# Kernel optimization log

Measured on AMD Instinct MI355X. Metric: run time of the kernel, lower is better.

The kernel has to match this reference:

```python
import jax, jax.numpy as jnp
import numpy as np


def _conv(x, w, pad):
    return jax.lax.conv_general_dilated(x, w, (1, 1), [(pad, pad), (pad, pad)],
                                        dimension_numbers=('NCHW', 'OIHW', 'NCHW'))


def _cbs(x, w, s, b, pad):
    # Conv + (folded inference BatchNorm as per-channel affine) + SiLU
    y = _conv(x, w, pad) * s[None, :, None, None] + b[None, :, None, None]
    return y * jax.nn.sigmoid(y)


def _pixel_shuffle(x, r):
    N, C, H, W = x.shape
    c = C // (r * r)
    return x.reshape(N, c, r, r, H, W).transpose(0, 1, 4, 2, 5, 3).reshape(N, c, H * r, W * r)


def _pixel_unshuffle(x, r):
    N, C, H, W = x.shape
    h, w = H // r, W // r
    return x.reshape(N, C, h, r, w, r).transpose(0, 1, 3, 5, 2, 4).reshape(N, C * r * r, h, w)


def _carafe(x, dw, db, ew, eb, k, up):
    # Content-aware reassembly: predict per-pixel k*k kernels for up*up sub-positions,
    # softmax-normalize, then gather-multiply-accumulate over k*k neighborhoods.
    N, C, H, W = x.shape
    kt = _conv(x, dw, 0) + db[None, :, None, None]
    if k % 2 == 0:
        kt = jnp.pad(kt, ((0, 0), (0, 0), (k // 2, k // 2 - 1), (k // 2, k // 2 - 1)))
        kt = _conv(kt, ew, 0) + eb[None, :, None, None]
    else:
        kt = _conv(kt, ew, k // 2) + eb[None, :, None, None]
    kt = _pixel_shuffle(kt, up)                     # [N, k*k, H*up, W*up]
    kt = jax.nn.softmax(kt, axis=1)
    # non-overlapping unfold(step=up) -> [N, H, W, k*k, up*up]
    kt = kt.reshape(N, k * k, H, up, W, up).transpose(0, 2, 4, 1, 3, 5).reshape(N, H, W, k * k, up * up)
    if k % 2 == 0:
        xp = jnp.pad(x, ((0, 0), (0, 0), (k // 2, k // 2 - 1), (k // 2, k // 2 - 1)))
    else:
        xp = jnp.pad(x, ((0, 0), (0, 0), (k // 2, k // 2), (k // 2, k // 2)))
    # k*k sliding patches (k is a small static constant)
    patches = jnp.stack([xp[:, :, i:i + H, j:j + W] for i in range(k) for j in range(k)], axis=-1)
    patches = patches.transpose(0, 2, 3, 1, 4)      # [N, H, W, C, k*k]
    out = jnp.einsum('nhwck,nhwkr->nhwcr', patches, kt)  # [N, H, W, C, up*up]
    out = out.reshape(N, H, W, C * up * up).transpose(0, 3, 1, 2)
    return _pixel_shuffle(out, up)


def _forward(x, cv1_w, cv1_s, cv1_b, m1a_w, m1a_s, m1a_b, m1b_w, m1b_s, m1b_b,
             cvm2_w, cvm2_s, cvm2_b, u2_down_w, u2_down_b, u2_enc_w, u2_enc_b,
             m2a_w, m2a_s, m2a_b, m2b_w, m2b_s, m2b_b,
             cvm3_w, cvm3_s, cvm3_b, u3_down_w, u3_down_b, u3_enc_w, u3_enc_b,
             m3a_w, m3a_s, m3a_b, m3b_w, m3b_s, m3b_b, cv2_w, cv2_s, cv2_b):
    C = cv1_w.shape[0] // 2
    t = _cbs(x, cv1_w, cv1_s, cv1_b, 0)
    y, y0 = t[:, :C], t[:, C:]

    def bneck(z, wa, sa, ba, wb, sb, bb):  # shortcut=False, e=1.0
        return _cbs(_cbs(z, wa, sa, ba, 1), wb, sb, bb, 1)

    y1 = bneck(y0, m1a_w, m1a_s, m1a_b, m1b_w, m1b_s, m1b_b)
    y2 = _cbs(_pixel_unshuffle(y1, 2), cvm2_w, cvm2_s, cvm2_b, 0)
    y2 = _carafe(y2, u2_down_w, u2_down_b, u2_enc_w, u2_enc_b, 1, 2) + y1
    y2 = bneck(y2, m2a_w, m2a_s, m2a_b, m2b_w, m2b_s, m2b_b)
    y3 = _cbs(_pixel_unshuffle(y2, 4), cvm3_w, cvm3_s, cvm3_b, 0)
    y3 = _carafe(y3, u3_down_w, u3_down_b, u3_enc_w, u3_enc_b, 2, 4) + y2
    y3 = bneck(y3, m3a_w, m3a_s, m3a_b, m3b_w, m3b_s, m3b_b)
    return _cbs(jnp.concatenate([y, y0, y1, y2, y3], axis=1), cv2_w, cv2_s, cv2_b, 0)


def setup_inputs() -> dict:
    key = jax.random.key(0)
    ks = jax.random.split(key, 16)
    C = 128

    def cbs_p(k, co, ci, ksz):
        k1, k2, k3 = jax.random.split(k, 3)
        w = jax.random.normal(k1, (co, ci, ksz, ksz), jnp.float32) / np.sqrt(ci * ksz * ksz).astype(np.float32)
        s = 1.0 + 0.1 * jax.random.normal(k2, (co,), jnp.float32)
        b = 0.1 * jax.random.normal(k3, (co,), jnp.float32)
        return w, s, b

    d = {}
    d['x'] = jax.random.normal(ks[0], (8, 256, 128, 128), jnp.float32)
    d['cv1_w'], d['cv1_s'], d['cv1_b'] = cbs_p(ks[1], 2 * C, 256, 1)
    for name, kk in (('m1', ks[2]), ('m2', ks[3]), ('m3', ks[4])):
        ka, kb = jax.random.split(kk)
        d[name + 'a_w'], d[name + 'a_s'], d[name + 'a_b'] = cbs_p(ka, C, C, 3)
        d[name + 'b_w'], d[name + 'b_s'], d[name + 'b_b'] = cbs_p(kb, C, C, 3)
    d['cvm2_w'], d['cvm2_s'], d['cvm2_b'] = cbs_p(ks[5], C, 4 * C, 1)
    d['cvm3_w'], d['cvm3_s'], d['cvm3_b'] = cbs_p(ks[6], C, 16 * C, 1)
    d['u2_down_w'] = jax.random.normal(ks[7], (C // 4, C, 1, 1), jnp.float32) / np.sqrt(C).astype(np.float32)
    d['u2_down_b'] = 0.1 * jax.random.normal(ks[8], (C // 4,), jnp.float32)
    d['u2_enc_w'] = jax.random.normal(ks[9], (4, C // 4, 1, 1), jnp.float32) / np.sqrt(C // 4).astype(np.float32)
    d['u2_enc_b'] = 0.1 * jax.random.normal(ks[10], (4,), jnp.float32)
    d['u3_down_w'] = jax.random.normal(ks[11], (C // 4, C, 1, 1), jnp.float32) / np.sqrt(C).astype(np.float32)
    d['u3_down_b'] = 0.1 * jax.random.normal(ks[12], (C // 4,), jnp.float32)
    d['u3_enc_w'] = jax.random.normal(ks[13], (64, C // 4, 2, 2), jnp.float32) / np.sqrt((C // 4) * 4).astype(np.float32)
    d['u3_enc_b'] = 0.1 * jax.random.normal(ks[14], (64,), jnp.float32)
    d['cv2_w'], d['cv2_s'], d['cv2_b'] = cbs_p(ks[15], 256, 5 * C, 1)
    return d


def reference(x, cv1_w, cv1_s, cv1_b, m1a_w, m1a_s, m1a_b, m1b_w, m1b_s, m1b_b,
              cvm2_w, cvm2_s, cvm2_b, u2_down_w, u2_down_b, u2_enc_w, u2_enc_b,
              m2a_w, m2a_s, m2a_b, m2b_w, m2b_s, m2b_b,
              cvm3_w, cvm3_s, cvm3_b, u3_down_w, u3_down_b, u3_enc_w, u3_enc_b,
              m3a_w, m3a_s, m3a_b, m3b_w, m3b_s, m3b_b, cv2_w, cv2_s, cv2_b):
    return _forward(x, cv1_w, cv1_s, cv1_b, m1a_w, m1a_s, m1a_b, m1b_w, m1b_s, m1b_b,
                    cvm2_w, cvm2_s, cvm2_b, u2_down_w, u2_down_b, u2_enc_w, u2_enc_b,
                    m2a_w, m2a_s, m2a_b, m2b_w, m2b_s, m2b_b,
                    cvm3_w, cvm3_s, cvm3_b, u3_down_w, u3_down_b, u3_enc_w, u3_enc_b,
                    m3a_w, m3a_s, m3a_b, m3b_w, m3b_s, m3b_b, cv2_w, cv2_s, cv2_b)
```

## Files before the change

kernel.cpp:

```cpp
#include <hip/hip_runtime.h>

typedef unsigned short u16;
typedef short v8s __attribute__((ext_vector_type(8)));
typedef u16 v8u __attribute__((ext_vector_type(8)));
typedef float v4f __attribute__((ext_vector_type(4)));
typedef __bf16 v8bf __attribute__((ext_vector_type(8)));

__device__ __forceinline__ float bf2f(u16 u) {
    unsigned x = ((unsigned)u) << 16; float f; __builtin_memcpy(&f, &x, 4); return f;
}
__device__ __forceinline__ u16 f2bf(float f) {
    unsigned x; __builtin_memcpy(&x, &f, 4);
    x = x + 0x7FFFu + ((x >> 16) & 1u);
    return (u16)(x >> 16);
}
__device__ __forceinline__ float silu(float v) { return v / (1.f + __expf(-v)); }

__device__ __forceinline__ void gld16(const void* g, void* l) {
    __builtin_amdgcn_global_load_lds(
        (const __attribute__((address_space(1))) unsigned int*)(uintptr_t)g,
        (__attribute__((address_space(3))) unsigned int*)(unsigned int)(uintptr_t)l,
        16, 0, 0);
}

__global__ void cvtw(const float* __restrict__ in, u16* __restrict__ out, int n) {
    int i = blockIdx.x * 256 + threadIdx.x;
    if (i < n) out[i] = f2bf(in[i]);
}
__global__ void wtrans3(const float* __restrict__ in, u16* __restrict__ out) {
    int i = blockIdx.x * 256 + threadIdx.x;
    if (i >= 147456) return;
    int tap = i % 9; int rem = i / 9; int ci = rem & 127; int co = rem >> 7;
    out[((tap * 128 + co) << 7) + ci] = f2bf(in[i]);
}
__global__ void wtrans_ps(const float* __restrict__ in, u16* __restrict__ out, int R2) {
    int i = blockIdx.x * 256 + threadIdx.x;
    int tap = i % R2; int rem = i / R2; int c = rem & 127; int co = rem >> 7;
    out[((tap * 128 + co) << 7) + c] = f2bf(in[i]);
}

__global__ __launch_bounds__(256) void nchw2nhwc(const float* __restrict__ in, u16* __restrict__ out) {
    __shared__ u16 tile[64][72];
    const int n = blockIdx.z, c0 = blockIdx.y * 64, p0 = blockIdx.x * 64;
#pragma unroll
    for (int rep = 0; rep < 16; ++rep) {
        int idx = rep * 256 + threadIdx.x;
        int c = idx >> 6, p = idx & 63;
        tile[c][p] = f2bf(in[((size_t)(n * 256 + c0 + c)) * 16384 + p0 + p]);
    }
    __syncthreads();
#pragma unroll
    for (int rep = 0; rep < 16; ++rep) {
        int idx = rep * 256 + threadIdx.x;
        int p = idx >> 6, c = idx & 63;
        out[((size_t)n * 16384 + p0 + p) * 256 + c0 + c] = tile[c][p];
    }
}

__global__ __launch_bounds__(256) void conv3_mfma(
    const u16* __restrict__ src, int c0, int srcC,
    const u16* __restrict__ wt,
    const float* __restrict__ scale, const float* __restrict__ bias,
    u16* __restrict__ out) {
    __shared__ u16 lds[3][128][32];
    const int n = blockIdx.y, h = blockIdx.x;
    const int tid = threadIdx.x;
    const int lane = tid & 63;
    const int wv = tid >> 6;
    const int r = lane & 15, q = lane >> 4;
    const int wr = wv >> 1, wc = wv & 1;

    v4f acc[4][4];
#pragma unroll
    for (int a = 0; a < 4; ++a)
#pragma unroll
        for (int b = 0; b < 4; ++b) acc[a][b] = (v4f){0.f, 0.f, 0.f, 0.f};

    const size_t rowstride = (size_t)128 * srcC;
    const u16* nbase = src + (size_t)n * 128 * rowstride + c0;

    for (int k0 = 0; k0 < 128; k0 += 32) {
        __syncthreads();
#pragma unroll
        for (int kh = 0; kh < 3; ++kh) {
            int hh = h + kh - 1;
            if ((unsigned)hh < 128u) {
                const u16* g = nbase + (size_t)hh * rowstride + k0;
#pragma unroll
                for (int j = 0; j < 2; ++j) {
                    int o = j * 4096 + tid * 16;
                    int px = o >> 6, cb = o & 63;
                    gld16((const char*)(g + (size_t)px * srcC) + cb,
                          (char*)&lds[kh][0][0] + j * 4096 + wv * 1024);
                }
            }
        }
        __syncthreads();
#pragma unroll
        for (int kh = 0; kh < 3; ++kh) {
            int hh = h + kh - 1;
            if ((unsigned)hh >= 128u) continue;
#pragma unroll
            for (int kw = 0; kw < 3; ++kw) {
                int tap = kh * 3 + kw;
                const u16* bb = wt + ((size_t)tap * 128 + wc * 64 + r) * 128 + k0 + q * 8;
                v8bf bfr[4];
#pragma unroll
                for (int nt = 0; nt < 4; ++nt)
                    bfr[nt] = __builtin_bit_cast(v8bf, *(const v8s*)(bb + nt * 16 * 128));
                v8bf afr[4];
#pragma unroll
                for (int mt = 0; mt < 4; ++mt) {
                    int p = wr * 64 + mt * 16 + r + kw - 1;
                    bool vp = (unsigned)p < 128u;
                    int pc = vp ? p : 0;
                    v8s av = *(const v8s*)&lds[kh][pc][q * 8];
                    if (!vp) av = (v8s){0, 0, 0, 0, 0, 0, 0, 0};
                    afr[mt] = __builtin_bit_cast(v8bf, av);
                }
#pragma unroll
                for (int mt = 0; mt < 4; ++mt)
#pragma unroll
                    for (int nt = 0; nt < 4; ++nt)
                        acc[mt][nt] = __builtin_amdgcn_mfma_f32_16x16x32_bf16(
                            afr[mt], bfr[nt], acc[mt][nt], 0, 0, 0);
            }
        }
    }

    const size_t obase = ((size_t)n * 128 + h) * 128;
#pragma unroll
    for (int nt = 0; nt < 4; ++nt) {
        int co = wc * 64 + nt * 16 + r;
        float s = scale[co], bi = bias[co];
#pragma unroll
        for (int mt = 0; mt < 4; ++mt) {
            int p = wr * 64 + mt * 16 + q * 4;
#pragma unroll
            for (int i = 0; i < 4; ++i) {
                float v = acc[mt][nt][i] * s + bi;
                out[(obase + p + i) * 128 + co] = f2bf(silu(v));
            }
        }
    }
}

__global__ __launch_bounds__(256) void conv1_mfma(
    const u16* __restrict__ src, int srcC,
    const u16* __restrict__ wt,
    const float* __restrict__ scale, const float* __restrict__ bias,
    u16* __restrict__ out, int Cout) {
    __shared__ u16 lds[128][64];
    const int n = blockIdx.z, co0 = blockIdx.y * 128, px0 = blockIdx.x * 128;
    const int tid = threadIdx.x;
    const int lane = tid & 63, wv = tid >> 6;
    const int r = lane & 15, q = lane >> 4;
    const int wr = wv >> 1, wc = wv & 1;

    v4f acc[4][4];
#pragma unroll
    for (int a = 0; a < 4; ++a)
#pragma unroll
        for (int b = 0; b < 4; ++b) acc[a][b] = (v4f){0.f, 0.f, 0.f, 0.f};

    const u16* abase = src + ((size_t)n * 16384 + px0) * srcC;

    for (int k0 = 0; k0 < srcC; k0 += 64) {
        __syncthreads();
#pragma unroll
        for (int j = 0; j < 4; ++j) {
            int o = j * 4096 + tid * 16;
            int px = o >> 7, cb = o & 127;
            gld16((const char*)(abase + (size_t)px * srcC + k0) + cb,
                  (char*)&lds[0][0] + j * 4096 + wv * 1024);
        }
        __syncthreads();
#pragma unroll
        for (int s = 0; s < 2; ++s) {
            const u16* bb = wt + (size_t)(co0 + wc * 64 + r) * srcC + k0 + s * 32 + q * 8;
            v8bf bfr[4];
#pragma unroll
            for (int nt = 0; nt < 4; ++nt)
                bfr[nt] = __builtin_bit_cast(v8bf, *(const v8s*)(bb + (size_t)nt * 16 * srcC));
            v8bf afr[4];
#pragma unroll
            for (int mt = 0; mt < 4; ++mt)
                afr[mt] = __builtin_bit_cast(v8bf, *(const v8s*)&lds[wr * 64 + mt * 16 + r][s * 32 + q * 8]);
#pragma unroll
            for (int mt = 0; mt < 4; ++mt)
#pragma unroll
                for (int nt = 0; nt < 4; ++nt)
                    acc[mt][nt] = __builtin_amdgcn_mfma_f32_16x16x32_bf16(
                        afr[mt], bfr[nt], acc[mt][nt], 0, 0, 0);
        }
    }

#pragma unroll
    for (int nt = 0; nt < 4; ++nt) {
        int co = co0 + wc * 64 + nt * 16 + r;
        float s = scale[co], bi = bias[co];
#pragma unroll
        for (int mt = 0; mt < 4; ++mt) {
            int p = px0 + wr * 64 + mt * 16 + q * 4;
#pragma unroll
            for (int i = 0; i < 4; ++i) {
                float v = acc[mt][nt][i] * s + bi;
                out[((size_t)n * 16384 + p + i) * Cout + co] = f2bf(silu(v));
            }
        }
    }
}

__global__ __launch_bounds__(256) void cat_mfma(
    const u16* __restrict__ s0, const u16* __restrict__ s1,
    const u16* __restrict__ s2, const u16* __restrict__ s3,
    const u16* __restrict__ wt,
    const float* __restrict__ scale, const float* __restrict__ bias,
    float* __restrict__ out) {
    __shared__ u16 lds[128][64];
    const int n = blockIdx.z, co0 = blockIdx.y * 128, px0 = blockIdx.x * 128;
    const int tid = threadIdx.x;
    const int lane = tid & 63, wv = tid >> 6;
    const int r = lane & 15, q = lane >> 4;
    const int wr = wv >> 1, wc = wv & 1;

    v4f acc[4][4];
#pragma unroll
    for (int a = 0; a < 4; ++a)
#pragma unroll
        for (int b = 0; b < 4; ++b) acc[a][b] = (v4f){0.f, 0.f, 0.f, 0.f};

    const u16* srcs[4] = {s0, s1, s2, s3};
    const int sCq[4] = {256, 128, 128, 128};
    const int kbq[4] = {0, 256, 384, 512};

#pragma unroll
    for (int seg = 0; seg < 4; ++seg) {
        const int sc = sCq[seg];
        const u16* ab = srcs[seg] + ((size_t)n * 16384 + px0) * sc;
        for (int k0 = 0; k0 < sc; k0 += 64) {
            __syncthreads();
#pragma unroll
            for (int j = 0; j < 4; ++j) {
                int o = j * 4096 + tid * 16;
                int px = o >> 7, cb = o & 127;
                gld16((const char*)(ab + (size_t)px * sc + k0) + cb,
                      (char*)&lds[0][0] + j * 4096 + wv * 1024);
            }
            __syncthreads();
#pragma unroll
            for (int s = 0; s < 2; ++s) {
                const u16* bb = wt + (size_t)(co0 + wc * 64 + r) * 640 + kbq[seg] + k0 + s * 32 + q * 8;
                v8bf bfr[4];
#pragma unroll
                for (int nt = 0; nt < 4; ++nt)
                    bfr[nt] = __builtin_bit_cast(v8bf, *(const v8s*)(bb + nt * 16 * 640));
                v8bf afr[4];
#pragma unroll
                for (int mt = 0; mt < 4; ++mt)
                    afr[mt] = __builtin_bit_cast(v8bf, *(const v8s*)&lds[wr * 64 + mt * 16 + r][s * 32 + q * 8]);
#pragma unroll
                for (int mt = 0; mt < 4; ++mt)
#pragma unroll
                    for (int nt = 0; nt < 4; ++nt)
                        acc[mt][nt] = __builtin_amdgcn_mfma_f32_16x16x32_bf16(
                            afr[mt], bfr[nt], acc[mt][nt], 0, 0, 0);
            }
        }
    }

#pragma unroll
    for (int nt = 0; nt < 4; ++nt) {
        int co = co0 + wc * 64 + nt * 16 + r;
        float s = scale[co], bi = bias[co];
#pragma unroll
        for (int mt = 0; mt < 4; ++mt) {
            int p = px0 + wr * 64 + mt * 16 + q * 4;
            v4f o;
#pragma unroll
            for (int i = 0; i < 4; ++i) o[i] = silu(acc[mt][nt][i] * s + bi);
            *(v4f*)(out + (size_t)(n * 256 + co) * 16384 + p) = o;
        }
    }
}

template <int KH, int KW, int S, int PAD, int CIN>
__global__ __launch_bounds__(256) void conv_mfma(
    const u16* __restrict__ src, int c0, int srcC,
    const u16* __restrict__ wt,
    const float* __restrict__ scale, const float* __restrict__ bias,
    u16* __restrict__ out, int Hin, int Win, int Wout, int Cout) {
    const int n = blockIdx.z;
    const int co0 = blockIdx.y * 64;
    const int hw0 = blockIdx.x * 64;
    const int tid = threadIdx.x;
    const int lane = tid & 63, wv = tid >> 6;
    const int r = lane & 15, q = lane >> 4;
    const int wr = wv >> 1, wc = wv & 1;

    const int m0 = hw0 + wr * 32 + r;
    const int m1 = m0 + 16;
    const int h0 = m0 / Wout, w0 = m0 - h0 * Wout;
    const int h1 = m1 / Wout, w1 = m1 - h1 * Wout;

    v4f acc00 = {0.f, 0.f, 0.f, 0.f}, acc01 = {0.f, 0.f, 0.f, 0.f};
    v4f acc10 = {0.f, 0.f, 0.f, 0.f}, acc11 = {0.f, 0.f, 0.f, 0.f};

    const u16* b0base = wt + (size_t)(co0 + wc * 32 + r) * CIN + q * 8;
    const size_t wtap = (size_t)Cout * CIN;

    int tap = 0;
#pragma unroll
    for (int kh = 0; kh < KH; ++kh)
#pragma unroll
        for (int kw = 0; kw < KW; ++kw, ++tap) {
            int ih0 = h0 * S + kh - PAD, iw0 = w0 * S + kw - PAD;
            int ih1 = h1 * S + kh - PAD, iw1 = w1 * S + kw - PAD;
            bool v0 = ((unsigned)ih0 < (unsigned)Hin) & ((unsigned)iw0 < (unsigned)Win);
            bool v1 = ((unsigned)ih1 < (unsigned)Hin) & ((unsigned)iw1 < (unsigned)Win);
            int p0i = v0 ? (n * Hin + ih0) * Win + iw0 : 0;
            int p1i = v1 ? (n * Hin + ih1) * Win + iw1 : 0;
            const u16* a0 = src + (size_t)p0i * srcC + c0 + q * 8;
            const u16* a1 = src + (size_t)p1i * srcC + c0 + q * 8;
            const u16* b0 = b0base + (size_t)tap * wtap;
            const u16* b1 = b0 + (size_t)16 * CIN;
#pragma unroll
            for (int k = 0; k < CIN; k += 32) {
                v8s za = {0, 0, 0, 0, 0, 0, 0, 0};
                v8s a0s = za, a1s = za;
                if (v0) a0s = *(const v8s*)(a0 + k);
                if (v1) a1s = *(const v8s*)(a1 + k);
                v8s b0s = *(const v8s*)(b0 + k);
                v8s b1s = *(const v8s*)(b1 + k);
                v8bf af0 = __builtin_bit_cast(v8bf, a0s);
                v8bf af1 = __builtin_bit_cast(v8bf, a1s);
                v8bf bw0 = __builtin_bit_cast(v8bf, b0s);
                v8bf bw1 = __builtin_bit_cast(v8bf, b1s);
                acc00 = __builtin_amdgcn_mfma_f32_16x16x32_bf16(af0, bw0, acc00, 0, 0, 0);
                acc01 = __builtin_amdgcn_mfma_f32_16x16x32_bf16(af0, bw1, acc01, 0, 0, 0);
                acc10 = __builtin_amdgcn_mfma_f32_16x16x32_bf16(af1, bw0, acc10, 0, 0, 0);
                acc11 = __builtin_amdgcn_mfma_f32_16x16x32_bf16(af1, bw1, acc11, 0, 0, 0);
            }
        }

    const int HWo = gridDim.x * 64;
#pragma unroll
    for (int ct = 0; ct < 2; ++ct) {
        v4f av0 = ct ? acc01 : acc00;
        v4f av1 = ct ? acc11 : acc10;
        int co = co0 + wc * 32 + ct * 16 + r;
        float s = scale[co], bb = bias[co];
        int mb = hw0 + wr * 32 + q * 4;
#pragma unroll
        for (int i = 0; i < 4; ++i) {
            float x0 = av0[i] * s + bb;
            float x1 = av1[i] * s + bb;
            out[((size_t)n * HWo + mb + i) * Cout + co] = f2bf(silu(x0));
            out[((size_t)n * HWo + mb + 16 + i) * Cout + co] = f2bf(silu(x1));
        }
    }
}

__global__ __launch_bounds__(256) void k_upadd(const u16* __restrict__ y2a,
                                               const u16* __restrict__ y1,
                                               u16* __restrict__ out) {
    int t = blockIdx.x * 256 + threadIdx.x;
    int cg = t & 15; int pix = t >> 4;
    int n = pix >> 14; int p = pix & 16383; int ho = p >> 7; int wo = p & 127;
    const u16* a = y2a + ((size_t)((n * 64 + (ho >> 1)) * 64 + (wo >> 1))) * 128 + cg * 8;
    const u16* b = y1 + (size_t)pix * 128 + cg * 8;
    v8s av = *(const v8s*)a;
    v8s bv = *(const v8s*)b;
    v8u o;
#pragma unroll
    for (int e = 0; e < 8; ++e) o[e] = f2bf(bf2f((u16)av[e]) + bf2f((u16)bv[e]));
    *(v8u*)(out + (size_t)pix * 128 + cg * 8) = o;
}

__global__ __launch_bounds__(256) void k_u3down(const u16* __restrict__ y3a,
                                                const float* __restrict__ w,
                                                const float* __restrict__ b,
                                                float* __restrict__ ktA) {
    int t = blockIdx.x * 256 + threadIdx.x;
    int co = t & 31; int pix = t >> 5;
    const u16* xr = y3a + (size_t)pix * 128;
    const float* wr = w + (size_t)co * 128;
    float acc = b[co];
#pragma unroll 16
    for (int k = 0; k < 128; ++k) acc += bf2f(xr[k]) * wr[k];
    ktA[t] = acc;
}

__global__ __launch_bounds__(256) void k_u3enc(const float* __restrict__ ktA,
                                               const float* __restrict__ ew,
                                               const float* __restrict__ eb,
                                               float* __restrict__ wtsm) {
    int t = blockIdx.x * 256 + threadIdx.x;
    int r = t & 15; int pix = t >> 4;
    int n = pix >> 10; int hw = pix & 1023; int h = hw >> 5; int w = hw & 31;
    float v[4];
#pragma unroll
    for (int kk = 0; kk < 4; ++kk) {
        int co = kk * 16 + r;
        float acc = eb[co];
#pragma unroll
        for (int dh = 0; dh < 2; ++dh)
#pragma unroll
            for (int dw = 0; dw < 2; ++dw) {
                int hh = h - 1 + dh, ww = w - 1 + dw;
                if (hh < 0 || ww < 0) continue;
                const float* kp = ktA + ((size_t)((n * 32 + hh) * 32 + ww)) * 32;
                const float* wp = ew + (size_t)co * 128 + dh * 2 + dw;
                for (int ci = 0; ci < 32; ++ci) acc += kp[ci] * wp[ci * 4];
            }
        v[kk] = acc;
    }
    float mx = fmaxf(fmaxf(v[0], v[1]), fmaxf(v[2], v[3]));
    float e0 = __expf(v[0] - mx), e1 = __expf(v[1] - mx), e2 = __expf(v[2] - mx), e3 = __expf(v[3] - mx);
    float inv = 1.f / (e0 + e1 + e2 + e3);
    float* o = wtsm + (size_t)t * 4;
    o[0] = e0 * inv; o[1] = e1 * inv; o[2] = e2 * inv; o[3] = e3 * inv;
}

__global__ __launch_bounds__(256) void k_carafe(const u16* __restrict__ y3a,
                                                const float* __restrict__ wtsm,
                                                const u16* __restrict__ y2,
                                                u16* __restrict__ out) {
    int t = blockIdx.x * 256 + threadIdx.x;
    int cg = t & 15; int pix = t >> 4;
    int n = pix >> 14; int p = pix & 16383; int ho = p >> 7; int wo = p & 127;
    int h = ho >> 2, i = ho & 3, w = wo >> 2, j = wo & 3, r = i * 4 + j;
    const float* wv = wtsm + ((size_t)((n * 1024 + h * 32 + w) * 16 + r)) * 4;
    v8s yv = *(const v8s*)(y2 + (size_t)pix * 128 + cg * 8);
    float acc[8];
#pragma unroll
    for (int e = 0; e < 8; ++e) acc[e] = bf2f((u16)yv[e]);
#pragma unroll
    for (int kk = 0; kk < 4; ++kk) {
        int ki = kk >> 1, kj = kk & 1;
        int hh = h + ki - 1, ww = w + kj - 1;
        if (hh < 0 || ww < 0) continue;
        float wk = wv[kk];
        v8s sv = *(const v8s*)(y3a + ((size_t)((n * 32 + hh) * 32 + ww)) * 128 + cg * 8);
#pragma unroll
        for (int e = 0; e < 8; ++e) acc[e] += wk * bf2f((u16)sv[e]);
    }
    v8u o;
#pragma unroll
    for (int e = 0; e < 8; ++e) o[e] = f2bf(acc[e]);
    *(v8u*)(out + (size_t)pix * 128 + cg * 8) = o;
}

extern "C" void kernel_launch(void* const* d_in, const int* in_sizes, int n_in,
                              void* d_out, int out_size, void* d_ws, size_t ws_size,
                              hipStream_t stream) {
    const float* x     = (const float*)d_in[0];
    const float* cv1_w = (const float*)d_in[1];
    const float* cv1_s = (const float*)d_in[2];
    const float* cv1_b = (const float*)d_in[3];
    const float* m1a_w = (const float*)d_in[4];
    const float* m1a_s = (const float*)d_in[5];
    const float* m1a_b = (const float*)d_in[6];
    const float* m1b_w = (const float*)d_in[7];
    const float* m1b_s = (const float*)d_in[8];
    const float* m1b_b = (const float*)d_in[9];
    const float* m2a_w = (const float*)d_in[10];
    const float* m2a_s = (const float*)d_in[11];
    const float* m2a_b = (const float*)d_in[12];
    const float* m2b_w = (const float*)d_in[13];
    const float* m2b_s = (const float*)d_in[14];
    const float* m2b_b = (const float*)d_in[15];
    const float* m3a_w = (const float*)d_in[16];
    const float* m3a_s = (const float*)d_in[17];
    const float* m3a_b = (const float*)d_in[18];
    const float* m3b_w = (const float*)d_in[19];
    const float* m3b_s = (const float*)d_in[20];
    const float* m3b_b = (const float*)d_in[21];
    const float* cvm2_w = (const float*)d_in[22];
    const float* cvm2_s = (const float*)d_in[23];
    const float* cvm2_b = (const float*)d_in[24];
    const float* cvm3_w = (const float*)d_in[25];
    const float* cvm3_s = (const float*)d_in[26];
    const float* cvm3_b = (const float*)d_in[27];
    const float* u3_down_w = (const float*)d_in[32];
    const float* u3_down_b = (const float*)d_in[33];
    const float* u3_enc_w  = (const float*)d_in[34];
    const float* u3_enc_b  = (const float*)d_in[35];
    const float* cv2_w = (const float*)d_in[36];
    const float* cv2_s = (const float*)d_in[37];
    const float* cv2_b = (const float*)d_in[38];

    char* ws = (char*)d_ws;
    u16* A    = (u16*)(ws + 0);
    u16* t    = (u16*)(ws + 67108864);
    u16* y1   = (u16*)(ws + 134217728);
    u16* bt   = (u16*)(ws + 167772160);
    u16* te   = (u16*)(ws + 201326592);
    u16* y2a  = (u16*)(ws + 234881024);
    u16* y3a  = (u16*)(ws + 243269632);
    float* ktA = (float*)(ws + 245366784);
    float* wts = (float*)(ws + 246415360);
    u16* w3t  = (u16*)(ws + 248512512);
    u16* wu2  = (u16*)(ws + 250281984);
    u16* wu4  = (u16*)(ws + 250413056);
    u16* wc1  = (u16*)(ws + 250937344);
    u16* wc2  = (u16*)(ws + 251068416);
    u16* y2 = A;
    u16* y3 = A + 16777216;

    dim3 B(256);
    wtrans3<<<576, B, 0, stream>>>(m1a_w, w3t + 0 * 147456);
    wtrans3<<<576, B, 0, stream>>>(m1b_w, w3t + 1 * 147456);
    wtrans3<<<576, B, 0, stream>>>(m2a_w, w3t + 2 * 147456);
    wtrans3<<<576, B, 0, stream>>>(m2b_w, w3t + 3 * 147456);
    wtrans3<<<576, B, 0, stream>>>(m3a_w, w3t + 4 * 147456);
    wtrans3<<<576, B, 0, stream>>>(m3b_w, w3t + 5 * 147456);
    wtrans_ps<<<256, B, 0, stream>>>(cvm2_w, wu2, 4);
    wtrans_ps<<<1024, B, 0, stream>>>(cvm3_w, wu4, 16);
    cvtw<<<256, B, 0, stream>>>(cv1_w, wc1, 65536);
    cvtw<<<640, B, 0, stream>>>(cv2_w, wc2, 163840);

    nchw2nhwc<<<dim3(256, 4, 8), B, 0, stream>>>(x, A);

    conv1_mfma<<<dim3(128, 2, 8), B, 0, stream>>>(A, 256, wc1, cv1_s, cv1_b, t, 256);

    conv3_mfma<<<dim3(128, 8), B, 0, stream>>>(t, 128, 256, w3t + 0 * 147456, m1a_s, m1a_b, bt);
    conv3_mfma<<<dim3(128, 8), B, 0, stream>>>(bt, 0, 128, w3t + 1 * 147456, m1b_s, m1b_b, y1);

    conv_mfma<2, 2, 2, 0, 128><<<dim3(64, 2, 8), B, 0, stream>>>(
        y1, 0, 128, wu2, cvm2_s, cvm2_b, y2a, 128, 128, 64, 128);

    k_upadd<<<8192, B, 0, stream>>>(y2a, y1, te);

    conv3_mfma<<<dim3(128, 8), B, 0, stream>>>(te, 0, 128, w3t + 2 * 147456, m2a_s, m2a_b, bt);
    conv3_mfma<<<dim3(128, 8), B, 0, stream>>>(bt, 0, 128, w3t + 3 * 147456, m2b_s, m2b_b, y2);

    conv_mfma<4, 4, 4, 0, 128><<<dim3(16, 2, 8), B, 0, stream>>>(
        y2, 0, 128, wu4, cvm3_s, cvm3_b, y3a, 128, 128, 32, 128);

    k_u3down<<<1024, B, 0, stream>>>(y3a, u3_down_w, u3_down_b, ktA);
    k_u3enc<<<512, B, 0, stream>>>(ktA, u3_enc_w, u3_enc_b, wts);
    k_carafe<<<8192, B, 0, stream>>>(y3a, wts, y2, te);

    conv3_mfma<<<dim3(128, 8), B, 0, stream>>>(te, 0, 128, w3t + 4 * 147456, m3a_s, m3a_b, bt);
    conv3_mfma<<<dim3(128, 8), B, 0, stream>>>(bt, 0, 128, w3t + 5 * 147456, m3b_s, m3b_b, y3);

    cat_mfma<<<dim3(128, 2, 8), B, 0, stream>>>(t, y1, y2, y3, wc2, cv2_s, cv2_b, (float*)d_out);
}
```

Baseline: 1.383 ms.

## Double-buffer LDS tiles with XOR swizzle and prefetch weights in MFMA conv kernels

Adds double-buffered LDS staging to the 3x3, 1x1 and concat-conv MFMA kernels, so the next K-chunk's global-to-LDS load is issued while the current chunk is computed. LDS addresses get an XOR swizzle to avoid bank conflicts on fragment reads. The 3x3 kernel prefetches next-tap weights into registers, and out-of-range rows are zero-filled in LDS. This doubles LDS use and raises register pressure, and a launch-bounds occupancy hint is added. There is only one barrier per iteration, which could race when the next stage overwrites a buffer still being read.

```diff
diff --git a/kernel.cpp b/kernel.cpp
--- a/kernel.cpp
+++ b/kernel.cpp
@@ -57,12 +57,12 @@
     }
 }
 
-__global__ __launch_bounds__(256) void conv3_mfma(
+__global__ __launch_bounds__(256, 3) void conv3_mfma(
     const u16* __restrict__ src, int c0, int srcC,
     const u16* __restrict__ wt,
     const float* __restrict__ scale, const float* __restrict__ bias,
     u16* __restrict__ out) {
-    __shared__ u16 lds[3][128][32];
+    __shared__ u16 lds[2][3][128][32];
     const int n = blockIdx.y, h = blockIdx.x;
     const int tid = threadIdx.x;
     const int lane = tid & 63;
@@ -79,51 +79,72 @@
     const size_t rowstride = (size_t)128 * srcC;
     const u16* nbase = src + (size_t)n * 128 * rowstride + c0;
 
-    for (int k0 = 0; k0 < 128; k0 += 32) {
-        __syncthreads();
+    auto stage = [&](int buf, int k0) {
 #pragma unroll
         for (int kh = 0; kh < 3; ++kh) {
             int hh = h + kh - 1;
+            char* dst0 = (char*)&lds[buf][kh][0][0];
             if ((unsigned)hh < 128u) {
                 const u16* g = nbase + (size_t)hh * rowstride + k0;
 #pragma unroll
                 for (int j = 0; j < 2; ++j) {
                     int o = j * 4096 + tid * 16;
-                    int px = o >> 6, cb = o & 63;
+                    int s2 = o ^ ((o >> 3) & 0x70);
+                    int px = s2 >> 6, cb = s2 & 63;
                     gld16((const char*)(g + (size_t)px * srcC) + cb,
-                          (char*)&lds[kh][0][0] + j * 4096 + wv * 1024);
+                          dst0 + j * 4096 + wv * 1024);
                 }
-            }
-        }
+            } else {
+#pragma unroll
+                for (int j = 0; j < 2; ++j)
+                    *(v8s*)(dst0 + j * 4096 + tid * 16) = (v8s){0, 0, 0, 0, 0, 0, 0, 0};
+            }
+        }
+    };
+
+    stage(0, 0);
+    int buf = 0;
+    for (int k0 = 0; k0 < 128; k0 += 32, buf ^= 1) {
         __syncthreads();
-#pragma unroll
-        for (int kh = 0; kh < 3; ++kh) {
-            int hh = h + kh - 1;
-            if ((unsigned)hh >= 128u) continue;
-#pragma unroll
-            for (int kw = 0; kw < 3; ++kw) {
-                int tap = kh * 3 + kw;
-                const u16* bb = wt + ((size_t)tap * 128 + wc * 64 + r) * 128 + k0 + q * 8;
-                v8bf bfr[4];
+        if (k0 + 32 < 128) stage(buf ^ 1, k0 + 32);
+
+        const u16* wk = wt + (size_t)(wc * 64 + r) * 128 + k0 + q * 8;
+        v8bf bcur[4];
+#pragma unroll
+        for (int nt = 0; nt < 4; ++nt)
+            bcur[nt] = __builtin_bit_cast(v8bf, *(const v8s*)(wk + nt * 2048));
+
+#pragma unroll
+        for (int tap = 0; tap < 9; ++tap) {
+            const int kh = tap / 3, kw = tap % 3;
+            v8bf afr[4];
+#pragma unroll
+            for (int mt = 0; mt < 4; ++mt) {
+                int p = wr * 64 + mt * 16 + r + kw - 1;
+                bool vp = (unsigned)p < 128u;
+                int pc = vp ? p : 0;
+                int ba = pc * 64 + q * 16;
+                ba ^= (ba >> 3) & 0x70;
+                v8s av = *(const v8s*)((const char*)&lds[buf][kh][0][0] + ba);
+                if (!vp) av = (v8s){0, 0, 0, 0, 0, 0, 0, 0};
+                afr[mt] = __builtin_bit_cast(v8bf, av);
+            }
+            v8bf bnxt[4];
+            if (tap < 8) {
 #pragma unroll
                 for (int nt = 0; nt < 4; ++nt)
-                    bfr[nt] = __builtin_bit_cast(v8bf, *(const v8s*)(bb + nt * 16 * 128));
-                v8bf afr[4];
-#pragma unroll
-                for (int mt = 0; mt < 4; ++mt) {
-                    int p = wr * 64 + mt * 16 + r + kw - 1;
-                    bool vp = (unsigned)p < 128u;
-                    int pc = vp ? p : 0;
-                    v8s av = *(const v8s*)&lds[kh][pc][q * 8];
-                    if (!vp) av = (v8s){0, 0, 0, 0, 0, 0, 0, 0};
-                    afr[mt] = __builtin_bit_cast(v8bf, av);
-                }
-#pragma unroll
-                for (int mt = 0; mt < 4; ++mt)
-#pragma unroll
-                    for (int nt = 0; nt < 4; ++nt)
-                        acc[mt][nt] = __builtin_amdgcn_mfma_f32_16x16x32_bf16(
-                            afr[mt], bfr[nt], acc[mt][nt], 0, 0, 0);
+                    bnxt[nt] = __builtin_bit_cast(v8bf,
+                        *(const v8s*)(wk + (size_t)(tap + 1) * 16384 + nt * 2048));
+            }
+#pragma unroll
+            for (int mt = 0; mt < 4; ++mt)
+#pragma unroll
+                for (int nt = 0; nt < 4; ++nt)
+                    acc[mt][nt] = __builtin_amdgcn_mfma_f32_16x16x32_bf16(
+                        afr[mt], bcur[nt], acc[mt][nt], 0, 0, 0);
+            if (tap < 8) {
+#pragma unroll
+                for (int nt = 0; nt < 4; ++nt) bcur[nt] = bnxt[nt];
             }
         }
     }
@@ -150,7 +171,7 @@
     const u16* __restrict__ wt,
     const float* __restrict__ scale, const float* __restrict__ bias,
     u16* __restrict__ out, int Cout) {
-    __shared__ u16 lds[128][64];
+    __shared__ u16 lds[2][128][64];
     const int n = blockIdx.z, co0 = blockIdx.y * 128, px0 = blockIdx.x * 128;
     const int tid = threadIdx.x;
     const int lane = tid & 63, wv = tid >> 6;
@@ -165,33 +186,47 @@
 
     const u16* abase = src + ((size_t)n * 16384 + px0) * srcC;
 
-    for (int k0 = 0; k0 < srcC; k0 += 64) {
-        __syncthreads();
+    auto stage = [&](int buf, int k0) {
 #pragma unroll
         for (int j = 0; j < 4; ++j) {
             int o = j * 4096 + tid * 16;
-            int px = o >> 7, cb = o & 127;
+            int s2 = o ^ ((o >> 3) & 0x70);
+            int px = s2 >> 7, cb = s2 & 127;
             gld16((const char*)(abase + (size_t)px * srcC + k0) + cb,
-                  (char*)&lds[0][0] + j * 4096 + wv * 1024);
-        }
+                  (char*)&lds[buf][0][0] + j * 4096 + wv * 1024);
+        }
+    };
+
+    stage(0, 0);
+    int buf = 0;
+    for (int k0 = 0; k0 < srcC; k0 += 64, buf ^= 1) {
         __syncthreads();
+        if (k0 + 64 < srcC) stage(buf ^ 1, k0 + 64);
+
+        const u16* wrow = wt + (size_t)(co0 + wc * 64 + r) * srcC + k0 + q * 8;
+        v8bf bfr[2][4];
+#pragma unroll
+        for (int s = 0; s < 2; ++s)
+#pragma unroll
+            for (int nt = 0; nt < 4; ++nt)
+                bfr[s][nt] = __builtin_bit_cast(v8bf,
+                    *(const v8s*)(wrow + s * 32 + (size_t)nt * 16 * srcC));
 #pragma unroll
         for (int s = 0; s < 2; ++s) {
-            const u16* bb = wt + (size_t)(co0 + wc * 64 + r) * srcC + k0 + s * 32 + q * 8;
-            v8bf bfr[4];
-#pragma unroll
-            for (int nt = 0; nt < 4; ++nt)
-                bfr[nt] = __builtin_bit_cast(v8bf, *(const v8s*)(bb + (size_t)nt * 16 * srcC));
             v8bf afr[4];
 #pragma unroll
-            for (int mt = 0; mt < 4; ++mt)
-                afr[mt] = __builtin_bit_cast(v8bf, *(const v8s*)&lds[wr * 64 + mt * 16 + r][s * 32 + q * 8]);
+            for (int mt = 0; mt < 4; ++mt) {
+                int ba = (wr * 64 + mt * 16 + r) * 128 + s * 64 + q * 16;
+                ba ^= (ba >> 3) & 0x70;
+                afr[mt] = __builtin_bit_cast(v8bf,
+                    *(const v8s*)((const char*)&lds[buf][0][0] + ba));
+            }
 #pragma unroll
             for (int mt = 0; mt < 4; ++mt)
 #pragma unroll
                 for (int nt = 0; nt < 4; ++nt)
                     acc[mt][nt] = __builtin_amdgcn_mfma_f32_16x16x32_bf16(
-                        afr[mt], bfr[nt], acc[mt][nt], 0, 0, 0);
+                        afr[mt], bfr[s][nt], acc[mt][nt], 0, 0, 0);
         }
     }
 
@@ -217,7 +252,7 @@
     const u16* __restrict__ wt,
     const float* __restrict__ scale, const float* __restrict__ bias,
     float* __restrict__ out) {
-    __shared__ u16 lds[128][64];
+    __shared__ u16 lds[2][128][64];
     const int n = blockIdx.z, co0 = blockIdx.y * 128, px0 = blockIdx.x * 128;
     const int tid = threadIdx.x;
     const int lane = tid & 63, wv = tid >> 6;
@@ -233,39 +268,54 @@
     const u16* srcs[4] = {s0, s1, s2, s3};
     const int sCq[4] = {256, 128, 128, 128};
     const int kbq[4] = {0, 256, 384, 512};
-
-#pragma unroll
-    for (int seg = 0; seg < 4; ++seg) {
-        const int sc = sCq[seg];
+    const int segs[10] = {0, 0, 0, 0, 1, 1, 2, 2, 3, 3};
+    const int k0s[10] = {0, 64, 128, 192, 0, 64, 0, 64, 0, 64};
+
+    auto stage = [&](int buf, int c) {
+        int seg = segs[c]; int sc = sCq[seg]; int k0 = k0s[c];
         const u16* ab = srcs[seg] + ((size_t)n * 16384 + px0) * sc;
-        for (int k0 = 0; k0 < sc; k0 += 64) {
-            __syncthreads();
-#pragma unroll
-            for (int j = 0; j < 4; ++j) {
-                int o = j * 4096 + tid * 16;
-                int px = o >> 7, cb = o & 127;
-                gld16((const char*)(ab + (size_t)px * sc + k0) + cb,
-                      (char*)&lds[0][0] + j * 4096 + wv * 1024);
-            }
-            __syncthreads();
-#pragma unroll
-            for (int s = 0; s < 2; ++s) {
-                const u16* bb = wt + (size_t)(co0 + wc * 64 + r) * 640 + kbq[seg] + k0 + s * 32 + q * 8;
-                v8bf bfr[4];
+#pragma unroll
+        for (int j = 0; j < 4; ++j) {
+            int o = j * 4096 + tid * 16;
+            int s2 = o ^ ((o >> 3) & 0x70);
+            int px = s2 >> 7, cb = s2 & 127;
+            gld16((const char*)(ab + (size_t)px * sc + k0) + cb,
+                  (char*)&lds[buf][0][0] + j * 4096 + wv * 1024);
+        }
+    };
+
+    stage(0, 0);
+    int buf = 0;
+#pragma unroll
+    for (int c = 0; c < 10; ++c, buf ^= 1) {
+        __syncthreads();
+        if (c < 9) stage(buf ^ 1, c + 1);
+
+        const int seg = segs[c], k0 = k0s[c];
+        const u16* wrow = wt + (size_t)(co0 + wc * 64 + r) * 640 + kbq[seg] + k0 + q * 8;
+        v8bf bfr[2][4];
+#pragma unroll
+        for (int s = 0; s < 2; ++s)
+#pragma unroll
+            for (int nt = 0; nt < 4; ++nt)
+                bfr[s][nt] = __builtin_bit_cast(v8bf,
+                    *(const v8s*)(wrow + s * 32 + (size_t)nt * 16 * 640));
+#pragma unroll
+        for (int s = 0; s < 2; ++s) {
+            v8bf afr[4];
+#pragma unroll
+            for (int mt = 0; mt < 4; ++mt) {
+                int ba = (wr * 64 + mt * 16 + r) * 128 + s * 64 + q * 16;
+                ba ^= (ba >> 3) & 0x70;
+                afr[mt] = __builtin_bit_cast(v8bf,
+                    *(const v8s*)((const char*)&lds[buf][0][0] + ba));
+            }
+#pragma unroll
+            for (int mt = 0; mt < 4; ++mt)
 #pragma unroll
                 for (int nt = 0; nt < 4; ++nt)
-                    bfr[nt] = __builtin_bit_cast(v8bf, *(const v8s*)(bb + nt * 16 * 640));
-                v8bf afr[4];
-#pragma unroll
-                for (int mt = 0; mt < 4; ++mt)
-                    afr[mt] = __builtin_bit_cast(v8bf, *(const v8s*)&lds[wr * 64 + mt * 16 + r][s * 32 + q * 8]);
-#pragma unroll
-                for (int mt = 0; mt < 4; ++mt)
-#pragma unroll
-                    for (int nt = 0; nt < 4; ++nt)
-                        acc[mt][nt] = __builtin_amdgcn_mfma_f32_16x16x32_bf16(
-                            afr[mt], bfr[nt], acc[mt][nt], 0, 0, 0);
-            }
+                    acc[mt][nt] = __builtin_amdgcn_mfma_f32_16x16x32_bf16(
+                        afr[mt], bfr[s][nt], acc[mt][nt], 0, 0, 0);
         }
     }
 
```

After: 1.378 ms. No clear change (-0.4%).
